# Kernel optimization log

Hardware: AMD Instinct MI355X
Metric: run time of the kernel (lower is better)

## Reference

```python
import jax, jax.numpy as jnp
import numpy as np

B, T, F, H = 64, 512, 512, 1024


def setup_inputs() -> dict:
    key = jax.random.key(0)
    k1, k2, k3 = jax.random.split(key, 3)
    x = jax.random.normal(k1, (B, T, F), dtype=jnp.float32)
    c0 = jnp.zeros((B, H), dtype=jnp.float32)
    h0 = jnp.zeros((B, H), dtype=jnp.float32)
    # Flax LSTMCell: input projection (no bias) + hidden projection (with bias),
    # fused here into [4H]-wide kernels with gate order (i, f, g, o).
    Wi = jax.random.normal(k2, (F, 4 * H), dtype=jnp.float32) / np.sqrt(F)
    Wh = jax.random.normal(k3, (H, 4 * H), dtype=jnp.float32) / np.sqrt(H)
    bh = jnp.zeros((4 * H,), dtype=jnp.float32)
    return {"x": x, "c0": c0, "h0": h0, "Wi": Wi, "Wh": Wh, "bh": bh}


def reference(x, c0, h0, Wi, Wh, bh):
    # Precompute input projections for the whole sequence in one big GEMM.
    # zx: (T, B, 4H)
    zx = jnp.einsum('btf,fg->tbg', x, Wi)

    def step(carry, zx_t):
        c, h = carry
        z = zx_t + h @ Wh + bh  # (B, 4H)
        i, f, g, o = jnp.split(z, 4, axis=-1)
        i = jax.nn.sigmoid(i)
        f = jax.nn.sigmoid(f)
        g = jnp.tanh(g)
        o = jax.nn.sigmoid(o)
        c_new = f * c + i * g
        h_new = o * jnp.tanh(c_new)
        return (c_new, h_new), h_new

    (_, _), ys = jax.lax.scan(step, (c0, h0), zx)
    return jnp.swapaxes(ys, 0, 1)  # (B, T, H)
```

## Files before the change

### kernel.cpp

```cpp
#include <hip/hip_runtime.h>

#define Bdim 64
#define Tdim 512
#define Fdim 512
#define Hdim 1024
#define NKB  48
#define NXKB 16
#define NHKB 32
#define NWG  128
#define NTHR 256

typedef __attribute__((ext_vector_type(8))) _Float16            f16x8;
typedef __attribute__((ext_vector_type(4))) float               f32x4;

#define MFMA(a, b, c) __builtin_amdgcn_mfma_f32_16x16x32_f16((a), (b), (c), 0, 0, 0)

#define WP_ELEMS  (256*48*64*8)
#define BIAS_OFF  ((size_t)WP_ELEMS * 2)
#define HBUF_OFF  (BIAS_OFF + 4096 * 4)
#define HBUF_HALF 65536
#define FLAG_OFF  (HBUF_OFF + (size_t)2 * HBUF_HALF * 2)
#define FLAG_STRIDE 32

__device__ __forceinline__ float sigmoidf_(float v) {
    return 1.0f / (1.0f + __expf(-v));
}
__device__ __forceinline__ float tanhf_(float v) {
    return 1.0f - 2.0f / (1.0f + __expf(2.0f * v));
}

__device__ __forceinline__ f16x8 uload16(const void* p) {
    f16x8 r;
    asm volatile("global_load_dwordx4 %0, %1, off sc0 sc1"
                 : "=v"(r) : "v"(p) : "memory");
    return r;
}

__global__ void pack_w_kernel(const float* __restrict__ Wi, const float* __restrict__ Wh,
                              _Float16* __restrict__ Wp)
{
    int d = blockIdx.x * blockDim.x + threadIdx.x;
    int tn   = d / 3072;
    int r    = d % 3072;
    int kb   = r / 64;
    int lane = r % 64;
    int kg = lane >> 4, lm = lane & 15;
    int Np = tn * 16 + lm;
    int g    = Np >> 5;
    int lc   = Np & 31;
    int gate = lc >> 3, c = lc & 7;
    int n  = gate * Hdim + g * 8 + c;
    int k0 = kb * 32 + kg * 8;
    f16x8 v;
#pragma unroll
    for (int j = 0; j < 8; ++j) {
        int k = k0 + j;
        float w = (k < Fdim) ? Wi[(long)k * 4096 + n] : Wh[(long)(k - Fdim) * 4096 + n];
        v[j] = (_Float16)w;
    }
    ((f16x8*)Wp)[d] = v;
}

__global__ void pack_misc_kernel(const float* __restrict__ bh, const float* __restrict__ h0,
                                 float* __restrict__ bias_p, _Float16* __restrict__ hbuf,
                                 unsigned int* __restrict__ flags)
{
    int t = blockIdx.x * blockDim.x + threadIdx.x;
    if (t < NWG) flags[t * FLAG_STRIDE] = 0u;
    if (t < 4096) {
        int g = t >> 5, lc = t & 31;
        int gate = lc >> 3, c = lc & 7;
        bias_p[t] = bh[gate * Hdim + g * 8 + c];
    }
    {
        int wgp = t >> 9;
        int b   = (t >> 3) & 63;
        int c   = t & 7;
        hbuf[t] = (_Float16)h0[b * Hdim + wgp * 8 + c];
    }
}

__global__ __launch_bounds__(NTHR, 1)
void lstm_kernel(const float* __restrict__ x, const float* __restrict__ c0,
                 const f16x8* __restrict__ Wp8, const float* __restrict__ bias_p,
                 _Float16* __restrict__ hbuf, unsigned int* __restrict__ flags,
                 float* __restrict__ out)
{
    __shared__ f16x8 wlds[2 * NKB * 64];
    __shared__ float zlds[Bdim][33];

    const int wg   = (blockIdx.x & 7) * 16 + (blockIdx.x >> 3);
    const int tid  = threadIdx.x;
    const int wave = tid >> 6;
    const int lane = tid & 63;
    const int kg = lane >> 4;
    const int lm = lane & 15;

    {
        const f16x8* src = Wp8 + (size_t)wg * 2 * NKB * 64;
        for (int e = tid; e < 2 * NKB * 64; e += NTHR) wlds[e] = src[e];
    }

    const float bias0 = bias_p[wg * 32 + lm];
    const float bias1 = bias_p[wg * 32 + 16 + lm];

    float cc[8];
    if (wave == 0) {
#pragma unroll
        for (int c = 0; c < 8; ++c) cc[c] = c0[lane * Hdim + wg * 8 + c];
    }

    const int arow = wave * 16 + lm;
    const float* __restrict__ xrow = x + (size_t)arow * Tdim * Fdim + kg * 8;

    const char* __restrict__ hrdbase =
        (const char*)hbuf + (size_t)kg * 1024 + (size_t)arow * 16;

    __syncthreads();

    for (int t = 0; t < Tdim; ++t) {
        const int cur = t & 1;

        f32x4 acc0a = {bias0, bias0, bias0, bias0};
        f32x4 acc1a = {bias1, bias1, bias1, bias1};
        f32x4 acc0b = {0.f, 0.f, 0.f, 0.f};
        f32x4 acc1b = {0.f, 0.f, 0.f, 0.f};

        {
            const float* xt = xrow + (size_t)t * Fdim;
#pragma unroll 8
            for (int kb = 0; kb < NXKB; ++kb) {
                const f32x4* ap = (const f32x4*)(xt + kb * 32);
                f32x4 lo = ap[0];
                f32x4 hi = ap[1];
                f16x8 a;
#pragma unroll
                for (int j = 0; j < 4; ++j) { a[j] = (_Float16)lo[j]; a[4 + j] = (_Float16)hi[j]; }
                f16x8 bf0 = wlds[kb * 64 + lane];
                f16x8 bf1 = wlds[NKB * 64 + kb * 64 + lane];
                if (kb & 1) { acc0b = MFMA(a, bf0, acc0b); acc1b = MFMA(a, bf1, acc1b); }
                else        { acc0a = MFMA(a, bf0, acc0a); acc1a = MFMA(a, bf1, acc1a); }
            }
        }

        if (t && wave == 0) {
            const unsigned int gen = (unsigned int)t;
            while (true) {
                unsigned int f0 = __hip_atomic_load(flags + (size_t)lane * FLAG_STRIDE,
                                                    __ATOMIC_RELAXED, __HIP_MEMORY_SCOPE_AGENT);
                unsigned int f1 = __hip_atomic_load(flags + (size_t)(64 + lane) * FLAG_STRIDE,
                                                    __ATOMIC_RELAXED, __HIP_MEMORY_SCOPE_AGENT);
                if (__all(f0 >= gen && f1 >= gen)) break;
                __builtin_amdgcn_s_sleep(2);
            }
        }
        __syncthreads();

        f16x8 hfrag[NHKB];
        {
            const char* hq = hrdbase + (size_t)cur * (HBUF_HALF * 2);
#pragma unroll
            for (int kb = 0; kb < NHKB; ++kb)
                hfrag[kb] = uload16(hq + (size_t)kb * 4096);
        }
        asm volatile("s_waitcnt vmcnt(0)" ::: "memory");
        __builtin_amdgcn_sched_barrier(0);

#pragma unroll
        for (int kb = 0; kb < NHKB; ++kb) {
            f16x8 a   = hfrag[kb];
            f16x8 bf0 = wlds[(NXKB + kb) * 64 + lane];
            f16x8 bf1 = wlds[NKB * 64 + (NXKB + kb) * 64 + lane];
            if (kb & 1) { acc0b = MFMA(a, bf0, acc0b); acc1b = MFMA(a, bf1, acc1b); }
            else        { acc0a = MFMA(a, bf0, acc0a); acc1a = MFMA(a, bf1, acc1a); }
        }
        f32x4 z0 = acc0a + acc0b;
        f32x4 z1 = acc1a + acc1b;

        {
            int rbase = wave * 16 + kg * 4;
#pragma unroll
            for (int r = 0; r < 4; ++r) {
                zlds[rbase + r][lm]      = z0[r];
                zlds[rbase + r][16 + lm] = z1[r];
            }
        }
        __syncthreads();

        if (wave == 0) {
            const int b = lane;
            float hv[8];
#pragma unroll
            for (int c = 0; c < 8; ++c) {
                float ig = sigmoidf_(zlds[b][c]);
                float fg = sigmoidf_(zlds[b][8 + c]);
                float gg = tanhf_(zlds[b][16 + c]);
                float og = sigmoidf_(zlds[b][24 + c]);
                cc[c] = fg * cc[c] + ig * gg;
                hv[c] = og * tanhf_(cc[c]);
            }
            union { _Float16 h[8]; unsigned long long u[2]; } pk;
#pragma unroll
            for (int c = 0; c < 8; ++c) pk.h[c] = (_Float16)hv[c];
            unsigned long long* hst = (unsigned long long*)
                (hbuf + (size_t)(cur ^ 1) * HBUF_HALF + (size_t)wg * 512 + (size_t)b * 8);
            __hip_atomic_store(hst,     pk.u[0], __ATOMIC_RELAXED, __HIP_MEMORY_SCOPE_AGENT);
            __hip_atomic_store(hst + 1, pk.u[1], __ATOMIC_RELAXED, __HIP_MEMORY_SCOPE_AGENT);
            asm volatile("s_waitcnt vmcnt(0)" ::: "memory");
            if (lane == 0)
                __hip_atomic_store(flags + (size_t)wg * FLAG_STRIDE, (unsigned int)(t + 1),
                                   __ATOMIC_RELAXED, __HIP_MEMORY_SCOPE_AGENT);
            float* op = out + ((size_t)b * Tdim + t) * Hdim + wg * 8;
            f32x4 o0 = {hv[0], hv[1], hv[2], hv[3]};
            f32x4 o1 = {hv[4], hv[5], hv[6], hv[7]};
            *(f32x4*)op       = o0;
            *(f32x4*)(op + 4) = o1;
        }
    }
}

extern "C" void kernel_launch(void* const* d_in, const int* in_sizes, int n_in,
                              void* d_out, int out_size, void* d_ws, size_t ws_size,
                              hipStream_t stream)
{
    const float* x  = (const float*)d_in[0];
    const float* c0 = (const float*)d_in[1];
    const float* h0 = (const float*)d_in[2];
    const float* Wi = (const float*)d_in[3];
    const float* Wh = (const float*)d_in[4];
    const float* bh = (const float*)d_in[5];
    float* out = (float*)d_out;

    char* ws = (char*)d_ws;
    _Float16*     Wp     = (_Float16*)(ws);
    float*        bias_p = (float*)(ws + BIAS_OFF);
    _Float16*     hbuf   = (_Float16*)(ws + HBUF_OFF);
    unsigned int* flags  = (unsigned int*)(ws + FLAG_OFF);

    hipLaunchKernelGGL(pack_w_kernel,    dim3(3072), dim3(256), 0, stream, Wi, Wh, Wp);
    hipLaunchKernelGGL(pack_misc_kernel, dim3(256),  dim3(256), 0, stream, bh, h0, bias_p, hbuf, flags);
    hipLaunchKernelGGL(lstm_kernel, dim3(NWG), dim3(NTHR), 0, stream,
                       x, c0, (const f16x8*)Wp, bias_p, hbuf, flags, out);
}
```

Baseline: 3.889 ms.

## Pipeline h-fragment loads with MFMAs and spread gate math across all waves

The recurrent h loads are split into four groups of eight, with partial vmcnt waits so MFMAs on one group can overlap loads of the next instead of waiting for all 32 loads. The elementwise LSTM gate update, previously done by wave 0 alone, is distributed over all four waves, two columns per thread. Lane pairs then combine their h values via shuffle for the store, and the flag is published after a block barrier. This shortens the serial critical path of each timestep, at the cost of an extra barrier and more register juggling.

```diff
diff --git a/kernel.cpp b/kernel.cpp
--- a/kernel.cpp
+++ b/kernel.cpp
@@ -35,6 +35,9 @@
                  : "=v"(r) : "v"(p) : "memory");
     return r;
 }
+
+#define WAITV(N) do { asm volatile("s_waitcnt vmcnt(" #N ")" ::: "memory"); \
+                      __builtin_amdgcn_sched_barrier(0); } while (0)
 
 __global__ void pack_w_kernel(const float* __restrict__ Wi, const float* __restrict__ Wh,
                               _Float16* __restrict__ Wp)
@@ -104,11 +107,10 @@
     const float bias0 = bias_p[wg * 32 + lm];
     const float bias1 = bias_p[wg * 32 + 16 + lm];
 
-    float cc[8];
-    if (wave == 0) {
-#pragma unroll
-        for (int c = 0; c < 8; ++c) cc[c] = c0[lane * Hdim + wg * 8 + c];
-    }
+    const int grow = wave * 16 + (lane >> 2);
+    const int gjl  = (lane & 3) * 2;
+    float cc0 = c0[grow * Hdim + wg * 8 + gjl];
+    float cc1 = c0[grow * Hdim + wg * 8 + gjl + 1];
 
     const int arow = wave * 16 + lm;
     const float* __restrict__ xrow = x + (size_t)arow * Tdim * Fdim + kg * 8;
@@ -156,23 +158,40 @@
         }
         __syncthreads();
 
-        f16x8 hfrag[NHKB];
         {
             const char* hq = hrdbase + (size_t)cur * (HBUF_HALF * 2);
-#pragma unroll
-            for (int kb = 0; kb < NHKB; ++kb)
-                hfrag[kb] = uload16(hq + (size_t)kb * 4096);
-        }
-        asm volatile("s_waitcnt vmcnt(0)" ::: "memory");
-        __builtin_amdgcn_sched_barrier(0);
-
-#pragma unroll
-        for (int kb = 0; kb < NHKB; ++kb) {
-            f16x8 a   = hfrag[kb];
-            f16x8 bf0 = wlds[(NXKB + kb) * 64 + lane];
-            f16x8 bf1 = wlds[NKB * 64 + (NXKB + kb) * 64 + lane];
-            if (kb & 1) { acc0b = MFMA(a, bf0, acc0b); acc1b = MFMA(a, bf1, acc1b); }
-            else        { acc0a = MFMA(a, bf0, acc0a); acc1a = MFMA(a, bf1, acc1a); }
+            f16x8 hA[8], hB[8];
+            WAITV(0);
+
+#define HLOAD(BASE, H)                                                  \
+            _Pragma("unroll")                                           \
+            for (int k = 0; k < 8; ++k)                                 \
+                H[k] = uload16(hq + (size_t)((BASE) + k) * 4096);
+
+#define HGROUP(BASE, H)                                                 \
+            _Pragma("unroll")                                           \
+            for (int k = 0; k < 8; ++k) {                               \
+                int kb = (BASE) + k;                                    \
+                f16x8 bf0 = wlds[(NXKB + kb) * 64 + lane];              \
+                f16x8 bf1 = wlds[NKB * 64 + (NXKB + kb) * 64 + lane];   \
+                if (kb & 1) { acc0b = MFMA(H[k], bf0, acc0b); acc1b = MFMA(H[k], bf1, acc1b); } \
+                else        { acc0a = MFMA(H[k], bf0, acc0a); acc1a = MFMA(H[k], bf1, acc1a); } \
+            }
+
+            HLOAD(0,  hA);
+            HLOAD(8,  hB);
+            WAITV(8);
+            HGROUP(0,  hA);
+            HLOAD(16, hA);
+            WAITV(8);
+            HGROUP(8,  hB);
+            HLOAD(24, hB);
+            WAITV(8);
+            HGROUP(16, hA);
+            WAITV(0);
+            HGROUP(24, hB);
+#undef HLOAD
+#undef HGROUP
         }
         f32x4 z0 = acc0a + acc0b;
         f32x4 z1 = acc1a + acc1b;
@@ -185,36 +204,48 @@
                 zlds[rbase + r][16 + lm] = z1[r];
             }
         }
+        asm volatile("s_waitcnt lgkmcnt(0)" ::: "memory");
+        __builtin_amdgcn_sched_barrier(0);
+
+        float hv0, hv1;
+        {
+            float i0 = sigmoidf_(zlds[grow][gjl]);
+            float f0 = sigmoidf_(zlds[grow][8 + gjl]);
+            float g0 = tanhf_(zlds[grow][16 + gjl]);
+            float o0 = sigmoidf_(zlds[grow][24 + gjl]);
+            cc0 = f0 * cc0 + i0 * g0;
+            hv0 = o0 * tanhf_(cc0);
+
+            float i1 = sigmoidf_(zlds[grow][gjl + 1]);
+            float f1 = sigmoidf_(zlds[grow][8 + gjl + 1]);
+            float g1 = tanhf_(zlds[grow][16 + gjl + 1]);
+            float o1 = sigmoidf_(zlds[grow][24 + gjl + 1]);
+            cc1 = f1 * cc1 + i1 * g1;
+            hv1 = o1 * tanhf_(cc1);
+        }
+
+        {
+            union { _Float16 h[2]; unsigned int u; } pk;
+            pk.h[0] = (_Float16)hv0; pk.h[1] = (_Float16)hv1;
+            unsigned int nbu = __shfl(pk.u, lane ^ 1);
+            if (!(lane & 1)) {
+                unsigned long long v = (unsigned long long)pk.u
+                                     | ((unsigned long long)nbu << 32);
+                __hip_atomic_store((unsigned long long*)
+                    (hbuf + (size_t)(cur ^ 1) * HBUF_HALF + (size_t)wg * 512
+                          + (size_t)grow * 8 + gjl),
+                    v, __ATOMIC_RELAXED, __HIP_MEMORY_SCOPE_AGENT);
+            }
+        }
+        asm volatile("s_waitcnt vmcnt(0)" ::: "memory");
         __syncthreads();
-
-        if (wave == 0) {
-            const int b = lane;
-            float hv[8];
-#pragma unroll
-            for (int c = 0; c < 8; ++c) {
-                float ig = sigmoidf_(zlds[b][c]);
-                float fg = sigmoidf_(zlds[b][8 + c]);
-                float gg = tanhf_(zlds[b][16 + c]);
-                float og = sigmoidf_(zlds[b][24 + c]);
-                cc[c] = fg * cc[c] + ig * gg;
-                hv[c] = og * tanhf_(cc[c]);
-            }
-            union { _Float16 h[8]; unsigned long long u[2]; } pk;
-#pragma unroll
-            for (int c = 0; c < 8; ++c) pk.h[c] = (_Float16)hv[c];
-            unsigned long long* hst = (unsigned long long*)
-                (hbuf + (size_t)(cur ^ 1) * HBUF_HALF + (size_t)wg * 512 + (size_t)b * 8);
-            __hip_atomic_store(hst,     pk.u[0], __ATOMIC_RELAXED, __HIP_MEMORY_SCOPE_AGENT);
-            __hip_atomic_store(hst + 1, pk.u[1], __ATOMIC_RELAXED, __HIP_MEMORY_SCOPE_AGENT);
-            asm volatile("s_waitcnt vmcnt(0)" ::: "memory");
-            if (lane == 0)
-                __hip_atomic_store(flags + (size_t)wg * FLAG_STRIDE, (unsigned int)(t + 1),
-                                   __ATOMIC_RELAXED, __HIP_MEMORY_SCOPE_AGENT);
-            float* op = out + ((size_t)b * Tdim + t) * Hdim + wg * 8;
-            f32x4 o0 = {hv[0], hv[1], hv[2], hv[3]};
-            f32x4 o1 = {hv[4], hv[5], hv[6], hv[7]};
-            *(f32x4*)op       = o0;
-            *(f32x4*)(op + 4) = o1;
+        if (tid == 0)
+            __hip_atomic_store(flags + (size_t)wg * FLAG_STRIDE, (unsigned int)(t + 1),
+                               __ATOMIC_RELAXED, __HIP_MEMORY_SCOPE_AGENT);
+
+        {
+            float2 ov; ov.x = hv0; ov.y = hv1;
+            *(float2*)(out + ((size_t)grow * Tdim + t) * Hdim + wg * 8 + gjl) = ov;
         }
     }
 }
```

Measured after the change: 3.584 ms. 1.09x faster.
